# Performance work log

Measured on AMD Instinct MI355X. Metric: run time of the kernel, lower is better.

The kernel has to match this reference:

```python
import jax, jax.numpy as jnp
import numpy as np

E = 8        # num_experts
H = 2048     # hidden_size
I = 1408     # intermediate_size
K = 2        # top_k
B, S = 1, 2048


def setup_inputs() -> dict:
    key = jax.random.key(0)
    k1, k2, k3, k4, k5 = jax.random.split(key, 5)
    hidden_states = jax.random.normal(k1, (B, S, H), dtype=jnp.float32)
    top_k_index = jax.random.randint(k2, (B, S, K), 0, E, dtype=jnp.int32)
    top_k_weights = jax.random.uniform(k3, (B, S, K), dtype=jnp.float32)
    # scaled init so activations stay O(1)
    gate_up_proj = jax.random.normal(k4, (E, 2 * I, H), dtype=jnp.float32) / np.sqrt(H)
    down_proj = jax.random.normal(k5, (E, H, I), dtype=jnp.float32) / np.sqrt(I)
    return {
        "hidden_states": hidden_states,
        "top_k_index": top_k_index,
        "top_k_weights": top_k_weights,
        "gate_up_proj": gate_up_proj,
        "down_proj": down_proj,
    }


def reference(hidden_states, top_k_index, top_k_weights, gate_up_proj, down_proj):
    orig_shape = hidden_states.shape
    x = hidden_states.reshape(-1, H)            # [T, H]
    idx = top_k_index.reshape(-1, K)            # [T, K] int32
    w = top_k_weights.reshape(-1, K)            # [T, K]
    out = jnp.zeros_like(x)
    for e in range(E):
        # combine weight for tokens routed to expert e (0 if not routed)
        we = jnp.sum(w * (idx == e).astype(w.dtype), axis=-1)   # [T]
        gu = x @ gate_up_proj[e].T                              # [T, 2I]
        gate, up = gu[:, :I], gu[:, I:]
        h = jax.nn.silu(gate) * up                              # [T, I]
        y = h @ down_proj[e].T                                  # [T, H]
        out = out + we[:, None] * y
    return out.reshape(orig_shape)
```

## Files before the change

### kernel.cpp

```cpp
#include <hip/hip_runtime.h>
#include <hip/hip_bf16.h>

#define E_ 8
#define H_ 2048
#define I_ 1408
#define S_ 2048
#define NPAIR 4096
#define MAXMT 32

typedef short bf16x8 __attribute__((ext_vector_type(8)));
typedef ushort u16x8 __attribute__((ext_vector_type(8)));
typedef float f32x4  __attribute__((ext_vector_type(4)));

__device__ inline bf16x8 pack8(float4 a, float4 b) {
    bf16x8 r;
    const float v[8] = {a.x, a.y, a.z, a.w, b.x, b.y, b.z, b.w};
#pragma unroll
    for (int j = 0; j < 8; ++j) {
        __hip_bfloat16 t = __float2bfloat16(v[j]);
        r[j] = *reinterpret_cast<short*>(&t);
    }
    return r;
}

__global__ void moe_router(const int* __restrict__ idx,
                           int* __restrict__ counts, int* __restrict__ bases,
                           int* __restrict__ tok, int* __restrict__ inv) {
    __shared__ int cnt[E_];
    __shared__ int cur[E_];
    const int tid = threadIdx.x;
    if (tid < E_) cnt[tid] = 0;
    __syncthreads();
    for (int p = tid; p < NPAIR; p += 256)
        atomicAdd(&cnt[idx[p]], 1);
    __syncthreads();
    if (tid == 0) {
        int b = 0;
        for (int e = 0; e < E_; ++e) {
            counts[e] = cnt[e];
            bases[e]  = b;
            cur[e]    = b;
            b += cnt[e];
        }
    }
    __syncthreads();
    for (int p = tid; p < NPAIR; p += 256) {
        const int e = idx[p];
        const int pos = atomicAdd(&cur[e], 1);
        tok[pos] = p >> 1;
        inv[p]   = pos;
    }
}

__global__ void convert_x(const float* __restrict__ x, ushort* __restrict__ xb) {
    const size_t i = ((size_t)blockIdx.x * 256 + threadIdx.x) * 8;
    const float4 a = *(const float4*)(x + i);
    const float4 b = *(const float4*)(x + i + 4);
    *(bf16x8*)(xb + i) = pack8(a, b);
}

__global__ __launch_bounds__(256, 2)
void moe_gemm1(const ushort* __restrict__ xb,
               const float* __restrict__ wg,
               const int* __restrict__ counts,
               const int* __restrict__ bases,
               const int* __restrict__ tok,
               ushort* __restrict__ hbuf) {
    const int e  = blockIdx.y & (E_ - 1);
    const int mt = blockIdx.y >> 3;
    const int count = counts[e];
    if (mt * 128 >= count) return;
    const int base = bases[e];
    const int n0 = blockIdx.x * 128;
    const float* wge = wg + (size_t)e * (2 * I_) * H_;

    __shared__ alignas(16) ushort sm[2][3][5120];

    const int tid  = threadIdx.x;
    const int lane = tid & 63;
    const int wid  = tid >> 6;
    const int wm = wid & 1, wn = wid >> 1;
    const int lr = lane & 15, lq = lane >> 4;

    const f32x4 vzero = {0.f, 0.f, 0.f, 0.f};
    f32x4 accg[4][4], accu[4][4];
#pragma unroll
    for (int mi = 0; mi < 4; ++mi)
#pragma unroll
        for (int ni = 0; ni < 4; ++ni) { accg[mi][ni] = vzero; accu[mi][ni] = vzero; }

    const int srow = tid >> 2;
    const int sc8  = (tid & 3) * 8;
    const int r0 = srow, r1 = srow + 64;

    const int ia0 = mt * 128 + r0, ia1 = mt * 128 + r1;
    const bool v0 = ia0 < count, v1 = ia1 < count;
    const ushort* ap0 = xb + (size_t)(v0 ? tok[base + ia0] : 0) * H_ + sc8;
    const ushort* ap1 = xb + (size_t)(v1 ? tok[base + ia1] : 0) * H_ + sc8;
    const float* gp0 = wge + (size_t)(n0 + r0) * H_ + sc8;
    const float* gp1 = wge + (size_t)(n0 + r1) * H_ + sc8;
    const float* up0 = gp0 + (size_t)I_ * H_;
    const float* up1 = gp1 + (size_t)I_ * H_;

    const uint4 z4 = {0u, 0u, 0u, 0u};
    uint4 ra0, ra1;
    float4 rg0a, rg0b, rg1a, rg1b, ru0a, ru0b, ru1a, ru1b;

    ra0 = v0 ? *(const uint4*)ap0 : z4;
    ra1 = v1 ? *(const uint4*)ap1 : z4;
    rg0a = *(const float4*)gp0; rg0b = *(const float4*)(gp0 + 4);
    rg1a = *(const float4*)gp1; rg1b = *(const float4*)(gp1 + 4);
    ru0a = *(const float4*)up0; ru0b = *(const float4*)(up0 + 4);
    ru1a = *(const float4*)up1; ru1b = *(const float4*)(up1 + 4);
    {
        ushort* As = &sm[0][0][0]; ushort* Bg = &sm[0][1][0]; ushort* Bu = &sm[0][2][0];
        *(uint4*)&As[r0 * 40 + sc8] = ra0;
        *(uint4*)&As[r1 * 40 + sc8] = ra1;
        *(bf16x8*)&Bg[r0 * 40 + sc8] = pack8(rg0a, rg0b);
        *(bf16x8*)&Bg[r1 * 40 + sc8] = pack8(rg1a, rg1b);
        *(bf16x8*)&Bu[r0 * 40 + sc8] = pack8(ru0a, ru0b);
        *(bf16x8*)&Bu[r1 * 40 + sc8] = pack8(ru1a, ru1b);
    }
    __syncthreads();

    for (int kt = 0; kt < H_ / 32; ++kt) {
        const int cur = kt & 1;
        if (kt < H_ / 32 - 1) {
            ap0 += 32; ap1 += 32; gp0 += 32; gp1 += 32; up0 += 32; up1 += 32;
            ra0 = v0 ? *(const uint4*)ap0 : z4;
            ra1 = v1 ? *(const uint4*)ap1 : z4;
            rg0a = *(const float4*)gp0; rg0b = *(const float4*)(gp0 + 4);
            rg1a = *(const float4*)gp1; rg1b = *(const float4*)(gp1 + 4);
            ru0a = *(const float4*)up0; ru0b = *(const float4*)(up0 + 4);
            ru1a = *(const float4*)up1; ru1b = *(const float4*)(up1 + 4);
        }
        const ushort* As = &sm[cur][0][0];
        const ushort* Bg = &sm[cur][1][0];
        const ushort* Bu = &sm[cur][2][0];
        bf16x8 a[4], bg[4], bu[4];
#pragma unroll
        for (int mi = 0; mi < 4; ++mi)
            a[mi] = *(const bf16x8*)&As[(wm * 64 + mi * 16 + lr) * 40 + lq * 8];
#pragma unroll
        for (int ni = 0; ni < 4; ++ni) {
            bg[ni] = *(const bf16x8*)&Bg[(wn * 64 + ni * 16 + lr) * 40 + lq * 8];
            bu[ni] = *(const bf16x8*)&Bu[(wn * 64 + ni * 16 + lr) * 40 + lq * 8];
        }
#pragma unroll
        for (int mi = 0; mi < 4; ++mi)
#pragma unroll
            for (int ni = 0; ni < 4; ++ni) {
                accg[mi][ni] = __builtin_amdgcn_mfma_f32_16x16x32_bf16(a[mi], bg[ni], accg[mi][ni], 0, 0, 0);
                accu[mi][ni] = __builtin_amdgcn_mfma_f32_16x16x32_bf16(a[mi], bu[ni], accu[mi][ni], 0, 0, 0);
            }
        if (kt < H_ / 32 - 1) {
            ushort* nA = &sm[cur ^ 1][0][0];
            ushort* nG = &sm[cur ^ 1][1][0];
            ushort* nU = &sm[cur ^ 1][2][0];
            *(uint4*)&nA[r0 * 40 + sc8] = ra0;
            *(uint4*)&nA[r1 * 40 + sc8] = ra1;
            *(bf16x8*)&nG[r0 * 40 + sc8] = pack8(rg0a, rg0b);
            *(bf16x8*)&nG[r1 * 40 + sc8] = pack8(rg1a, rg1b);
            *(bf16x8*)&nU[r0 * 40 + sc8] = pack8(ru0a, ru0b);
            *(bf16x8*)&nU[r1 * 40 + sc8] = pack8(ru1a, ru1b);
        }
        __syncthreads();
    }

    ushort* Ht = &sm[0][0][0];
#pragma unroll
    for (int mi = 0; mi < 4; ++mi)
#pragma unroll
        for (int r = 0; r < 4; ++r) {
            const int row = wm * 64 + mi * 16 + lq * 4 + r;
#pragma unroll
            for (int ni = 0; ni < 4; ++ni) {
                const int col = wn * 64 + ni * 16 + lr;
                const float g = accg[mi][ni][r];
                const float u = accu[mi][ni][r];
                const float h = (g / (1.0f + __expf(-g))) * u;
                __hip_bfloat16 hb = __float2bfloat16(h);
                Ht[row * 136 + col] = *reinterpret_cast<ushort*>(&hb);
            }
        }
    __syncthreads();
#pragma unroll
    for (int p = 0; p < 8; ++p) {
        const int slot = p * 256 + tid;
        const int row = slot >> 4;
        const int cc  = (slot & 15) * 8;
        const int gi = mt * 128 + row;
        if (gi < count)
            *(uint4*)&hbuf[(size_t)(base + gi) * I_ + n0 + cc] = *(const uint4*)&Ht[row * 136 + cc];
    }
}

__global__ __launch_bounds__(256, 2)
void moe_gemm2(const ushort* __restrict__ hbuf,
               const float* __restrict__ wd,
               const int* __restrict__ counts,
               const int* __restrict__ bases,
               ushort* __restrict__ ybuf) {
    const int e  = blockIdx.y & (E_ - 1);
    const int mt = blockIdx.y >> 3;
    const int count = counts[e];
    if (mt * 128 >= count) return;
    const int base = bases[e];
    const int n0 = blockIdx.x * 128;
    const float* wde = wd + (size_t)e * H_ * I_;

    __shared__ alignas(16) ushort sm[2][2][5120];

    const int tid  = threadIdx.x;
    const int lane = tid & 63;
    const int wid  = tid >> 6;
    const int wm = wid & 1, wn = wid >> 1;
    const int lr = lane & 15, lq = lane >> 4;

    const f32x4 vzero = {0.f, 0.f, 0.f, 0.f};
    f32x4 acc[4][4];
#pragma unroll
    for (int mi = 0; mi < 4; ++mi)
#pragma unroll
        for (int ni = 0; ni < 4; ++ni) acc[mi][ni] = vzero;

    const int srow = tid >> 2;
    const int sc8  = (tid & 3) * 8;
    const int r0 = srow, r1 = srow + 64;

    const int ia0 = mt * 128 + r0, ia1 = mt * 128 + r1;
    const bool v0 = ia0 < count, v1 = ia1 < count;
    const ushort* ap0 = hbuf + (size_t)(base + (v0 ? ia0 : 0)) * I_ + sc8;
    const ushort* ap1 = hbuf + (size_t)(base + (v1 ? ia1 : 0)) * I_ + sc8;
    const float* bp0 = wde + (size_t)(n0 + r0) * I_ + sc8;
    const float* bp1 = wde + (size_t)(n0 + r1) * I_ + sc8;

    const uint4 z4 = {0u, 0u, 0u, 0u};
    uint4 ra0, ra1;
    float4 rb0a, rb0b, rb1a, rb1b;

    ra0 = v0 ? *(const uint4*)ap0 : z4;
    ra1 = v1 ? *(const uint4*)ap1 : z4;
    rb0a = *(const float4*)bp0; rb0b = *(const float4*)(bp0 + 4);
    rb1a = *(const float4*)bp1; rb1b = *(const float4*)(bp1 + 4);
    {
        ushort* As = &sm[0][0][0]; ushort* Bs = &sm[0][1][0];
        *(uint4*)&As[r0 * 40 + sc8] = ra0;
        *(uint4*)&As[r1 * 40 + sc8] = ra1;
        *(bf16x8*)&Bs[r0 * 40 + sc8] = pack8(rb0a, rb0b);
        *(bf16x8*)&Bs[r1 * 40 + sc8] = pack8(rb1a, rb1b);
    }
    __syncthreads();

    for (int kt = 0; kt < I_ / 32; ++kt) {
        const int cur = kt & 1;
        if (kt < I_ / 32 - 1) {
            ap0 += 32; ap1 += 32; bp0 += 32; bp1 += 32;
            ra0 = v0 ? *(const uint4*)ap0 : z4;
            ra1 = v1 ? *(const uint4*)ap1 : z4;
            rb0a = *(const float4*)bp0; rb0b = *(const float4*)(bp0 + 4);
            rb1a = *(const float4*)bp1; rb1b = *(const float4*)(bp1 + 4);
        }
        const ushort* As = &sm[cur][0][0];
        const ushort* Bs = &sm[cur][1][0];
        bf16x8 a[4], b[4];
#pragma unroll
        for (int mi = 0; mi < 4; ++mi)
            a[mi] = *(const bf16x8*)&As[(wm * 64 + mi * 16 + lr) * 40 + lq * 8];
#pragma unroll
        for (int ni = 0; ni < 4; ++ni)
            b[ni] = *(const bf16x8*)&Bs[(wn * 64 + ni * 16 + lr) * 40 + lq * 8];
#pragma unroll
        for (int mi = 0; mi < 4; ++mi)
#pragma unroll
            for (int ni = 0; ni < 4; ++ni)
                acc[mi][ni] = __builtin_amdgcn_mfma_f32_16x16x32_bf16(a[mi], b[ni], acc[mi][ni], 0, 0, 0);
        if (kt < I_ / 32 - 1) {
            ushort* nA = &sm[cur ^ 1][0][0];
            ushort* nB = &sm[cur ^ 1][1][0];
            *(uint4*)&nA[r0 * 40 + sc8] = ra0;
            *(uint4*)&nA[r1 * 40 + sc8] = ra1;
            *(bf16x8*)&nB[r0 * 40 + sc8] = pack8(rb0a, rb0b);
            *(bf16x8*)&nB[r1 * 40 + sc8] = pack8(rb1a, rb1b);
        }
        __syncthreads();
    }

    ushort* Yt = &sm[0][0][0];
#pragma unroll
    for (int mi = 0; mi < 4; ++mi)
#pragma unroll
        for (int r = 0; r < 4; ++r) {
            const int row = wm * 64 + mi * 16 + lq * 4 + r;
#pragma unroll
            for (int ni = 0; ni < 4; ++ni) {
                const int col = wn * 64 + ni * 16 + lr;
                __hip_bfloat16 yb = __float2bfloat16(acc[mi][ni][r]);
                Yt[row * 136 + col] = *reinterpret_cast<ushort*>(&yb);
            }
        }
    __syncthreads();
#pragma unroll
    for (int p = 0; p < 8; ++p) {
        const int slot = p * 256 + tid;
        const int row = slot >> 4;
        const int cc  = (slot & 15) * 8;
        const int gi = mt * 128 + row;
        if (gi < count)
            *(uint4*)&ybuf[(size_t)(base + gi) * H_ + n0 + cc] = *(const uint4*)&Yt[row * 136 + cc];
    }
}

__global__ void moe_combine(const ushort* __restrict__ ybuf,
                            const int* __restrict__ inv,
                            const float* __restrict__ tkw,
                            float* __restrict__ out) {
    const int t = blockIdx.x;
    const int c8 = threadIdx.x * 8;
    const int p0 = inv[2 * t], p1 = inv[2 * t + 1];
    const float w0 = tkw[2 * t], w1 = tkw[2 * t + 1];
    const u16x8 y0 = *(const u16x8*)(ybuf + (size_t)p0 * H_ + c8);
    const u16x8 y1 = *(const u16x8*)(ybuf + (size_t)p1 * H_ + c8);
    float o[8];
#pragma unroll
    for (int j = 0; j < 8; ++j) {
        const unsigned f0 = ((unsigned)y0[j]) << 16;
        const unsigned f1 = ((unsigned)y1[j]) << 16;
        o[j] = w0 * __uint_as_float(f0) + w1 * __uint_as_float(f1);
    }
    float* dst = out + (size_t)t * H_ + c8;
    *(float4*)dst       = make_float4(o[0], o[1], o[2], o[3]);
    *(float4*)(dst + 4) = make_float4(o[4], o[5], o[6], o[7]);
}

extern "C" void kernel_launch(void* const* d_in, const int* in_sizes, int n_in,
                              void* d_out, int out_size, void* d_ws, size_t ws_size,
                              hipStream_t stream) {
    const float* x   = (const float*)d_in[0];
    const int*   tki = (const int*)d_in[1];
    const float* tkw = (const float*)d_in[2];
    const float* wg  = (const float*)d_in[3];
    const float* wd  = (const float*)d_in[4];
    float* out = (float*)d_out;

    char* p = (char*)d_ws;
    int* counts = (int*)p;  p += 32;
    int* bases  = (int*)p;  p += 32;
    int* tok    = (int*)p;  p += NPAIR * sizeof(int);
    int* inv    = (int*)p;  p += NPAIR * sizeof(int);
    ushort* xb   = (ushort*)p; p += (size_t)S_ * H_ * 2;
    ushort* hbuf = (ushort*)p; p += (size_t)NPAIR * I_ * 2;
    ushort* ybuf = (ushort*)p; p += (size_t)NPAIR * H_ * 2;

    convert_x<<<dim3((S_ * H_) / (256 * 8)), 256, 0, stream>>>(x, xb);
    moe_router<<<dim3(1), 256, 0, stream>>>(tki, counts, bases, tok, inv);
    moe_gemm1<<<dim3(I_ / 128, E_ * MAXMT), 256, 0, stream>>>(xb, wg, counts, bases, tok, hbuf);
    moe_gemm2<<<dim3(H_ / 128, E_ * MAXMT), 256, 0, stream>>>(hbuf, wd, counts, bases, ybuf);
    moe_combine<<<dim3(S_), 256, 0, stream>>>(ybuf, inv, tkw, out);
}
```

Measured before the change: 426.3 us.

## Load MFMA operands directly from global memory, dropping LDS staging in MoE GEMMs

```diff
diff --git a/kernel.cpp b/kernel.cpp
--- a/kernel.cpp
+++ b/kernel.cpp
@@ -59,7 +59,7 @@
     *(bf16x8*)(xb + i) = pack8(a, b);
 }
 
-__global__ __launch_bounds__(256, 2)
+__global__ __launch_bounds__(256, 3)
 void moe_gemm1(const ushort* __restrict__ xb,
                const float* __restrict__ wg,
                const int* __restrict__ counts,
@@ -71,10 +71,8 @@
     const int count = counts[e];
     if (mt * 128 >= count) return;
     const int base = bases[e];
-    const int n0 = blockIdx.x * 128;
+    const int n0 = blockIdx.x * 64;
     const float* wge = wg + (size_t)e * (2 * I_) * H_;
-
-    __shared__ alignas(16) ushort sm[2][3][5120];
 
     const int tid  = threadIdx.x;
     const int lane = tid & 63;
@@ -82,120 +80,96 @@
     const int wm = wid & 1, wn = wid >> 1;
     const int lr = lane & 15, lq = lane >> 4;
 
+    int aoff[4];
+#pragma unroll
+    for (int mi = 0; mi < 4; ++mi) {
+        const int i = mt * 128 + wm * 64 + mi * 16 + lr;
+        const int ic = i < count ? i : count - 1;
+        aoff[mi] = tok[base + ic] * H_ + lq * 8;
+    }
+    int boff[4];
+#pragma unroll
+    for (int gu = 0; gu < 2; ++gu)
+#pragma unroll
+        for (int ni = 0; ni < 2; ++ni) {
+            const int row = gu * I_ + n0 + wn * 32 + ni * 16 + lr;
+            boff[gu * 2 + ni] = row * H_ + lq * 8;
+        }
+
     const f32x4 vzero = {0.f, 0.f, 0.f, 0.f};
-    f32x4 accg[4][4], accu[4][4];
-#pragma unroll
-    for (int mi = 0; mi < 4; ++mi)
-#pragma unroll
-        for (int ni = 0; ni < 4; ++ni) { accg[mi][ni] = vzero; accu[mi][ni] = vzero; }
-
-    const int srow = tid >> 2;
-    const int sc8  = (tid & 3) * 8;
-    const int r0 = srow, r1 = srow + 64;
-
-    const int ia0 = mt * 128 + r0, ia1 = mt * 128 + r1;
-    const bool v0 = ia0 < count, v1 = ia1 < count;
-    const ushort* ap0 = xb + (size_t)(v0 ? tok[base + ia0] : 0) * H_ + sc8;
-    const ushort* ap1 = xb + (size_t)(v1 ? tok[base + ia1] : 0) * H_ + sc8;
-    const float* gp0 = wge + (size_t)(n0 + r0) * H_ + sc8;
-    const float* gp1 = wge + (size_t)(n0 + r1) * H_ + sc8;
-    const float* up0 = gp0 + (size_t)I_ * H_;
-    const float* up1 = gp1 + (size_t)I_ * H_;
-
-    const uint4 z4 = {0u, 0u, 0u, 0u};
-    uint4 ra0, ra1;
-    float4 rg0a, rg0b, rg1a, rg1b, ru0a, ru0b, ru1a, ru1b;
-
-    ra0 = v0 ? *(const uint4*)ap0 : z4;
-    ra1 = v1 ? *(const uint4*)ap1 : z4;
-    rg0a = *(const float4*)gp0; rg0b = *(const float4*)(gp0 + 4);
-    rg1a = *(const float4*)gp1; rg1b = *(const float4*)(gp1 + 4);
-    ru0a = *(const float4*)up0; ru0b = *(const float4*)(up0 + 4);
-    ru1a = *(const float4*)up1; ru1b = *(const float4*)(up1 + 4);
-    {
-        ushort* As = &sm[0][0][0]; ushort* Bg = &sm[0][1][0]; ushort* Bu = &sm[0][2][0];
-        *(uint4*)&As[r0 * 40 + sc8] = ra0;
-        *(uint4*)&As[r1 * 40 + sc8] = ra1;
-        *(bf16x8*)&Bg[r0 * 40 + sc8] = pack8(rg0a, rg0b);
-        *(bf16x8*)&Bg[r1 * 40 + sc8] = pack8(rg1a, rg1b);
-        *(bf16x8*)&Bu[r0 * 40 + sc8] = pack8(ru0a, ru0b);
-        *(bf16x8*)&Bu[r1 * 40 + sc8] = pack8(ru1a, ru1b);
-    }
-    __syncthreads();
-
-    for (int kt = 0; kt < H_ / 32; ++kt) {
-        const int cur = kt & 1;
-        if (kt < H_ / 32 - 1) {
-            ap0 += 32; ap1 += 32; gp0 += 32; gp1 += 32; up0 += 32; up1 += 32;
-            ra0 = v0 ? *(const uint4*)ap0 : z4;
-            ra1 = v1 ? *(const uint4*)ap1 : z4;
-            rg0a = *(const float4*)gp0; rg0b = *(const float4*)(gp0 + 4);
-            rg1a = *(const float4*)gp1; rg1b = *(const float4*)(gp1 + 4);
-            ru0a = *(const float4*)up0; ru0b = *(const float4*)(up0 + 4);
-            ru1a = *(const float4*)up1; ru1b = *(const float4*)(up1 + 4);
-        }
-        const ushort* As = &sm[cur][0][0];
-        const ushort* Bg = &sm[cur][1][0];
-        const ushort* Bu = &sm[cur][2][0];
-        bf16x8 a[4], bg[4], bu[4];
+    f32x4 acc[4][4];
+#pragma unroll
+    for (int f = 0; f < 4; ++f)
+#pragma unroll
+        for (int mi = 0; mi < 4; ++mi) acc[f][mi] = vzero;
+
+    bf16x8 a[4], b[4];
+    float4 bf[4][2];
+
+#pragma unroll
+    for (int mi = 0; mi < 4; ++mi) a[mi] = *(const bf16x8*)(xb + aoff[mi]);
+#pragma unroll
+    for (int f = 0; f < 4; ++f) {
+        bf[f][0] = *(const float4*)(wge + boff[f]);
+        bf[f][1] = *(const float4*)(wge + boff[f] + 4);
+    }
+
+#pragma unroll 1
+    for (int kt = 0; kt < H_ / 32 - 1; ++kt) {
+#pragma unroll
+        for (int f = 0; f < 4; ++f) b[f] = pack8(bf[f][0], bf[f][1]);
+        const float* bp = wge + (kt + 1) * 32;
+#pragma unroll
+        for (int f = 0; f < 4; ++f) {
+            bf[f][0] = *(const float4*)(bp + boff[f]);
+            bf[f][1] = *(const float4*)(bp + boff[f] + 4);
+        }
+#pragma unroll
+        for (int f = 0; f < 4; ++f)
+#pragma unroll
+            for (int mi = 0; mi < 4; ++mi)
+                acc[f][mi] = __builtin_amdgcn_mfma_f32_16x16x32_bf16(a[mi], b[f], acc[f][mi], 0, 0, 0);
+        const ushort* ap = xb + (kt + 1) * 32;
+#pragma unroll
+        for (int mi = 0; mi < 4; ++mi) a[mi] = *(const bf16x8*)(ap + aoff[mi]);
+    }
+#pragma unroll
+    for (int f = 0; f < 4; ++f) b[f] = pack8(bf[f][0], bf[f][1]);
+#pragma unroll
+    for (int f = 0; f < 4; ++f)
 #pragma unroll
         for (int mi = 0; mi < 4; ++mi)
-            a[mi] = *(const bf16x8*)&As[(wm * 64 + mi * 16 + lr) * 40 + lq * 8];
-#pragma unroll
-        for (int ni = 0; ni < 4; ++ni) {
-            bg[ni] = *(const bf16x8*)&Bg[(wn * 64 + ni * 16 + lr) * 40 + lq * 8];
-            bu[ni] = *(const bf16x8*)&Bu[(wn * 64 + ni * 16 + lr) * 40 + lq * 8];
-        }
-#pragma unroll
-        for (int mi = 0; mi < 4; ++mi)
-#pragma unroll
-            for (int ni = 0; ni < 4; ++ni) {
-                accg[mi][ni] = __builtin_amdgcn_mfma_f32_16x16x32_bf16(a[mi], bg[ni], accg[mi][ni], 0, 0, 0);
-                accu[mi][ni] = __builtin_amdgcn_mfma_f32_16x16x32_bf16(a[mi], bu[ni], accu[mi][ni], 0, 0, 0);
-            }
-        if (kt < H_ / 32 - 1) {
-            ushort* nA = &sm[cur ^ 1][0][0];
-            ushort* nG = &sm[cur ^ 1][1][0];
-            ushort* nU = &sm[cur ^ 1][2][0];
-            *(uint4*)&nA[r0 * 40 + sc8] = ra0;
-            *(uint4*)&nA[r1 * 40 + sc8] = ra1;
-            *(bf16x8*)&nG[r0 * 40 + sc8] = pack8(rg0a, rg0b);
-            *(bf16x8*)&nG[r1 * 40 + sc8] = pack8(rg1a, rg1b);
-            *(bf16x8*)&nU[r0 * 40 + sc8] = pack8(ru0a, ru0b);
-            *(bf16x8*)&nU[r1 * 40 + sc8] = pack8(ru1a, ru1b);
-        }
-        __syncthreads();
-    }
-
-    ushort* Ht = &sm[0][0][0];
+            acc[f][mi] = __builtin_amdgcn_mfma_f32_16x16x32_bf16(a[mi], b[f], acc[f][mi], 0, 0, 0);
+
+    __shared__ alignas(16) ushort Ht[128 * 72];
 #pragma unroll
     for (int mi = 0; mi < 4; ++mi)
 #pragma unroll
         for (int r = 0; r < 4; ++r) {
             const int row = wm * 64 + mi * 16 + lq * 4 + r;
 #pragma unroll
-            for (int ni = 0; ni < 4; ++ni) {
-                const int col = wn * 64 + ni * 16 + lr;
-                const float g = accg[mi][ni][r];
-                const float u = accu[mi][ni][r];
+            for (int ni = 0; ni < 2; ++ni) {
+                const int col = wn * 32 + ni * 16 + lr;
+                const float g = acc[ni][mi][r];
+                const float u = acc[2 + ni][mi][r];
                 const float h = (g / (1.0f + __expf(-g))) * u;
                 __hip_bfloat16 hb = __float2bfloat16(h);
-                Ht[row * 136 + col] = *reinterpret_cast<ushort*>(&hb);
+                Ht[row * 72 + col] = *reinterpret_cast<ushort*>(&hb);
             }
         }
     __syncthreads();
 #pragma unroll
-    for (int p = 0; p < 8; ++p) {
+    for (int p = 0; p < 4; ++p) {
         const int slot = p * 256 + tid;
-        const int row = slot >> 4;
-        const int cc  = (slot & 15) * 8;
+        const int row = slot >> 3;
+        const int cc  = (slot & 7) * 8;
         const int gi = mt * 128 + row;
         if (gi < count)
-            *(uint4*)&hbuf[(size_t)(base + gi) * I_ + n0 + cc] = *(const uint4*)&Ht[row * 136 + cc];
-    }
-}
-
-__global__ __launch_bounds__(256, 2)
+            *(uint4*)&hbuf[(size_t)(base + gi) * I_ + n0 + cc] = *(const uint4*)&Ht[row * 72 + cc];
+    }
+}
+
+__global__ __launch_bounds__(256, 3)
 void moe_gemm2(const ushort* __restrict__ hbuf,
                const float* __restrict__ wd,
                const int* __restrict__ counts,
@@ -209,84 +183,72 @@
     const int n0 = blockIdx.x * 128;
     const float* wde = wd + (size_t)e * H_ * I_;
 
-    __shared__ alignas(16) ushort sm[2][2][5120];
-
     const int tid  = threadIdx.x;
     const int lane = tid & 63;
     const int wid  = tid >> 6;
     const int wm = wid & 1, wn = wid >> 1;
     const int lr = lane & 15, lq = lane >> 4;
 
+    int aoff[4];
+#pragma unroll
+    for (int mi = 0; mi < 4; ++mi) {
+        const int i = mt * 128 + wm * 64 + mi * 16 + lr;
+        const int ic = i < count ? i : count - 1;
+        aoff[mi] = (base + ic) * I_ + lq * 8;
+    }
+    int boff[4];
+#pragma unroll
+    for (int ni = 0; ni < 4; ++ni) {
+        const int row = n0 + wn * 64 + ni * 16 + lr;
+        boff[ni] = row * I_ + lq * 8;
+    }
+
     const f32x4 vzero = {0.f, 0.f, 0.f, 0.f};
     f32x4 acc[4][4];
 #pragma unroll
-    for (int mi = 0; mi < 4; ++mi)
-#pragma unroll
-        for (int ni = 0; ni < 4; ++ni) acc[mi][ni] = vzero;
-
-    const int srow = tid >> 2;
-    const int sc8  = (tid & 3) * 8;
-    const int r0 = srow, r1 = srow + 64;
-
-    const int ia0 = mt * 128 + r0, ia1 = mt * 128 + r1;
-    const bool v0 = ia0 < count, v1 = ia1 < count;
-    const ushort* ap0 = hbuf + (size_t)(base + (v0 ? ia0 : 0)) * I_ + sc8;
-    const ushort* ap1 = hbuf + (size_t)(base + (v1 ? ia1 : 0)) * I_ + sc8;
-    const float* bp0 = wde + (size_t)(n0 + r0) * I_ + sc8;
-    const float* bp1 = wde + (size_t)(n0 + r1) * I_ + sc8;
-
-    const uint4 z4 = {0u, 0u, 0u, 0u};
-    uint4 ra0, ra1;
-    float4 rb0a, rb0b, rb1a, rb1b;
-
-    ra0 = v0 ? *(const uint4*)ap0 : z4;
-    ra1 = v1 ? *(const uint4*)ap1 : z4;
-    rb0a = *(const float4*)bp0; rb0b = *(const float4*)(bp0 + 4);
-    rb1a = *(const float4*)bp1; rb1b = *(const float4*)(bp1 + 4);
-    {
-        ushort* As = &sm[0][0][0]; ushort* Bs = &sm[0][1][0];
-        *(uint4*)&As[r0 * 40 + sc8] = ra0;
-        *(uint4*)&As[r1 * 40 + sc8] = ra1;
-        *(bf16x8*)&Bs[r0 * 40 + sc8] = pack8(rb0a, rb0b);
-        *(bf16x8*)&Bs[r1 * 40 + sc8] = pack8(rb1a, rb1b);
-    }
-    __syncthreads();
-
-    for (int kt = 0; kt < I_ / 32; ++kt) {
-        const int cur = kt & 1;
-        if (kt < I_ / 32 - 1) {
-            ap0 += 32; ap1 += 32; bp0 += 32; bp1 += 32;
-            ra0 = v0 ? *(const uint4*)ap0 : z4;
-            ra1 = v1 ? *(const uint4*)ap1 : z4;
-            rb0a = *(const float4*)bp0; rb0b = *(const float4*)(bp0 + 4);
-            rb1a = *(const float4*)bp1; rb1b = *(const float4*)(bp1 + 4);
-        }
-        const ushort* As = &sm[cur][0][0];
-        const ushort* Bs = &sm[cur][1][0];
-        bf16x8 a[4], b[4];
+    for (int ni = 0; ni < 4; ++ni)
+#pragma unroll
+        for (int mi = 0; mi < 4; ++mi) acc[ni][mi] = vzero;
+
+    bf16x8 a[4], b[4];
+    float4 bf[4][2];
+
+#pragma unroll
+    for (int mi = 0; mi < 4; ++mi) a[mi] = *(const bf16x8*)(hbuf + aoff[mi]);
+#pragma unroll
+    for (int ni = 0; ni < 4; ++ni) {
+        bf[ni][0] = *(const float4*)(wde + boff[ni]);
+        bf[ni][1] = *(const float4*)(wde + boff[ni] + 4);
+    }
+
+#pragma unroll 1
+    for (int kt = 0; kt < I_ / 32 - 1; ++kt) {
+#pragma unroll
+        for (int ni = 0; ni < 4; ++ni) b[ni] = pack8(bf[ni][0], bf[ni][1]);
+        const float* bp = wde + (kt + 1) * 32;
+#pragma unroll
+        for (int ni = 0; ni < 4; ++ni) {
+            bf[ni][0] = *(const float4*)(bp + boff[ni]);
+            bf[ni][1] = *(const float4*)(bp + boff[ni] + 4);
+        }
+#pragma unroll
+        for (int ni = 0; ni < 4; ++ni)
+#pragma unroll
+            for (int mi = 0; mi < 4; ++mi)
+                acc[ni][mi] = __builtin_amdgcn_mfma_f32_16x16x32_bf16(a[mi], b[ni], acc[ni][mi], 0, 0, 0);
+        const ushort* ap = hbuf + (kt + 1) * 32;
+#pragma unroll
+        for (int mi = 0; mi < 4; ++mi) a[mi] = *(const bf16x8*)(ap + aoff[mi]);
+    }
+#pragma unroll
+    for (int ni = 0; ni < 4; ++ni) b[ni] = pack8(bf[ni][0], bf[ni][1]);
+#pragma unroll
+    for (int ni = 0; ni < 4; ++ni)
 #pragma unroll
         for (int mi = 0; mi < 4; ++mi)
-            a[mi] = *(const bf16x8*)&As[(wm * 64 + mi * 16 + lr) * 40 + lq * 8];
-#pragma unroll
-        for (int ni = 0; ni < 4; ++ni)
-            b[ni] = *(const bf16x8*)&Bs[(wn * 64 + ni * 16 + lr) * 40 + lq * 8];
-#pragma unroll
-        for (int mi = 0; mi < 4; ++mi)
-#pragma unroll
-            for (int ni = 0; ni < 4; ++ni)
-                acc[mi][ni] = __builtin_amdgcn_mfma_f32_16x16x32_bf16(a[mi], b[ni], acc[mi][ni], 0, 0, 0);
-        if (kt < I_ / 32 - 1) {
-            ushort* nA = &sm[cur ^ 1][0][0];
-            ushort* nB = &sm[cur ^ 1][1][0];
-            *(uint4*)&nA[r0 * 40 + sc8] = ra0;
-            *(uint4*)&nA[r1 * 40 + sc8] = ra1;
-            *(bf16x8*)&nB[r0 * 40 + sc8] = pack8(rb0a, rb0b);
-            *(bf16x8*)&nB[r1 * 40 + sc8] = pack8(rb1a, rb1b);
-        }
-        __syncthreads();
-    }
-
-    ushort* Yt = &sm[0][0][0];
+            acc[ni][mi] = __builtin_amdgcn_mfma_f32_16x16x32_bf16(a[mi], b[ni], acc[ni][mi], 0, 0, 0);
+
+    __shared__ alignas(16) ushort Yt[128 * 136];
 #pragma unroll
     for (int mi = 0; mi < 4; ++mi)
 #pragma unroll
@@ -295,7 +257,7 @@
 #pragma unroll
             for (int ni = 0; ni < 4; ++ni) {
                 const int col = wn * 64 + ni * 16 + lr;
-                __hip_bfloat16 yb = __float2bfloat16(acc[mi][ni][r]);
+                __hip_bfloat16 yb = __float2bfloat16(acc[ni][mi][r]);
                 Yt[row * 136 + col] = *reinterpret_cast<ushort*>(&yb);
             }
         }
@@ -354,7 +316,7 @@
 
     convert_x<<<dim3((S_ * H_) / (256 * 8)), 256, 0, stream>>>(x, xb);
     moe_router<<<dim3(1), 256, 0, stream>>>(tki, counts, bases, tok, inv);
-    moe_gemm1<<<dim3(I_ / 128, E_ * MAXMT), 256, 0, stream>>>(xb, wg, counts, bases, tok, hbuf);
+    moe_gemm1<<<dim3(I_ / 64, E_ * MAXMT), 256, 0, stream>>>(xb, wg, counts, bases, tok, hbuf);
     moe_gemm2<<<dim3(H_ / 128, E_ * MAXMT), 256, 0, stream>>>(hbuf, wd, counts, bases, ybuf);
     moe_combine<<<dim3(S_), 256, 0, stream>>>(ybuf, inv, tkw, out);
 }
```

Result: slower. 813.9 us (+90.9%).
